# Optimization experiments

Hardware: AMD Instinct MI355X
Metric: run time of the kernel (lower is better)

Reference implementation:

```python
import jax, jax.numpy as jnp
import numpy as np

TOPK = 2
ALPHA_AUX = 0.02

def setup_inputs() -> dict:
    key = jax.random.key(0)
    ks = jax.random.split(key, 6)
    B, T, D, E, H = 2, 2048, 1024, 16, 1536
    s_in = 1.0 / np.sqrt(D)
    s_h = 1.0 / np.sqrt(H)
    return {
        "x": jax.random.normal(ks[0], (B, T, D), dtype=jnp.float32),
        "router_w": jax.random.normal(ks[1], (E, D), dtype=jnp.float32) * s_in,
        "w1": jax.random.normal(ks[2], (E, H, D), dtype=jnp.float32) * s_in,
        "b1": jax.random.normal(ks[3], (E, H), dtype=jnp.float32) * 0.01,
        "w2": jax.random.normal(ks[4], (E, D, H), dtype=jnp.float32) * s_h,
        "b2": jax.random.normal(ks[5], (E, D), dtype=jnp.float32) * 0.01,
    }

def reference(x, router_w, w1, b1, w2, b2):
    B, T, D = x.shape
    E = router_w.shape[0]
    N = B * T
    x_flat = x.reshape(N, D)

    # Router: top-k logits -> softmax gates -> dense dispatch matrix [N, E]
    logits = x_flat @ router_w.T                      # [N, E]
    vals, idx = jax.lax.top_k(logits, TOPK)           # [N, K]
    gate = jax.nn.softmax(vals, axis=-1)              # [N, K]
    rows = jnp.arange(N)[:, None]
    dispatch = jnp.zeros((N, E), dtype=x.dtype).at[rows, idx].set(gate)

    # Expert MLPs computed densely over all experts; gate==0 masks unselected,
    # reproducing the gather-MLP-scatter math exactly.
    h = jnp.einsum('nd,ehd->neh', x_flat, w1) + b1    # [N, E, H]
    h = jax.nn.gelu(h, approximate=True)              # tanh GELU
    y = jnp.einsum('neh,edh->ned', h, w2) + b2        # [N, E, D]
    out = jnp.einsum('ne,ned->nd', dispatch, y).reshape(B, T, D)

    # Auxiliary load-balancing loss
    tok_per_expert = (dispatch > 0).sum(0).astype(jnp.float32)  # [E]
    f_i = tok_per_expert / tok_per_expert.sum()
    m_i = dispatch.sum(0) / jnp.clip(tok_per_expert, 1.0, None)
    aux_loss = ALPHA_AUX * (f_i * m_i).mean()
    return out, aux_loss
```

## Files before the change

### kernel.cpp

```cpp
#include <hip/hip_runtime.h>
#include <hip/hip_bf16.h>
#include <math.h>

#define N_TOK 4096
#define DIM   1024
#define NEXP  16
#define HID   1536
#define TOPK2 2
#define NASSIGN (N_TOK * TOPK2)

#define MAX_ITEMS 80

typedef __attribute__((ext_vector_type(8))) short short8;
typedef __attribute__((ext_vector_type(4))) float floatx4;
typedef unsigned short u16;

#define GLOAD_LDS16(gp, lp)                                                     \
    __builtin_amdgcn_global_load_lds(                                           \
        (const __attribute__((address_space(1))) unsigned int*)(gp),            \
        (__attribute__((address_space(3))) unsigned int*)(lp), 16, 0, 0)

__global__ void cvt_kernel(const float* __restrict__ src, u16* __restrict__ dst, int n4) {
    int i = blockIdx.x * 256 + threadIdx.x;
    if (i >= n4) return;
    float4 v = ((const float4*)src)[i];
    __hip_bfloat16 a = __float2bfloat16(v.x), b = __float2bfloat16(v.y);
    __hip_bfloat16 c = __float2bfloat16(v.z), d = __float2bfloat16(v.w);
    ushort4 o;
    o.x = *(u16*)&a; o.y = *(u16*)&b; o.z = *(u16*)&c; o.w = *(u16*)&d;
    ((ushort4*)dst)[i] = o;
}

__global__ __launch_bounds__(256)
void logits_topk_kernel(const float* __restrict__ x, const float* __restrict__ rw,
                        int* __restrict__ idx, float* __restrict__ gate,
                        u16* __restrict__ x_bf) {
    int tb = blockIdx.x * 16;
    __shared__ float xs[16][68];
    __shared__ float rs[16][68];
    __shared__ float lg[16][17];

    int tid = threadIdx.x;
    int t = tid >> 4, e = tid & 15;
    int srow = tid >> 4, scol = (tid & 15) * 4;

    float acc = 0.f;
    for (int k0 = 0; k0 < DIM; k0 += 64) {
        float4 xv = *(const float4*)&x[(size_t)(tb + srow) * DIM + k0 + scol];
        *(float4*)&xs[srow][scol] = xv;
        *(float4*)&rs[srow][scol] = *(const float4*)&rw[(size_t)srow * DIM + k0 + scol];
        {
            __hip_bfloat16 a = __float2bfloat16(xv.x), b = __float2bfloat16(xv.y);
            __hip_bfloat16 c = __float2bfloat16(xv.z), d = __float2bfloat16(xv.w);
            ushort4 o;
            o.x = *(u16*)&a; o.y = *(u16*)&b; o.z = *(u16*)&c; o.w = *(u16*)&d;
            *(ushort4*)&x_bf[(size_t)(tb + srow) * DIM + k0 + scol] = o;
        }
        __syncthreads();
        const float2* xp = (const float2*)xs[t];
        const float2* rp = (const float2*)rs[e];
        #pragma unroll
        for (int k = 0; k < 32; k++) {
            float2 a = xp[k], b = rp[k];
            acc = fmaf(a.x, b.x, acc);
            acc = fmaf(a.y, b.y, acc);
        }
        __syncthreads();
    }
    lg[t][e] = acc;
    __syncthreads();

    if (tid < 16) {
        int n = tb + tid;
        float v0 = -3.402823466e+38f, v1 = -3.402823466e+38f;
        int i0 = 0, i1 = 0;
        #pragma unroll
        for (int ee = 0; ee < NEXP; ee++) {
            float v = lg[tid][ee];
            if (v > v0) { v1 = v0; i1 = i0; v0 = v; i0 = ee; }
            else if (v > v1) { v1 = v; i1 = ee; }
        }
        float e1 = expf(v1 - v0);
        float inv = 1.f / (1.f + e1);
        idx[2 * n] = i0; idx[2 * n + 1] = i1;
        gate[2 * n] = inv; gate[2 * n + 1] = e1 * inv;
    }
}

__global__ __launch_bounds__(256)
void plan_kernel(const int* __restrict__ idx, const float* __restrict__ gate,
                 int* __restrict__ offsets, int* __restrict__ tlist,
                 int* __restrict__ wl, int* __restrict__ wcount,
                 float* __restrict__ aux_out) {
    __shared__ int cnt_s[16];
    __shared__ float gs_s[16];
    __shared__ int pos_s[16];
    __shared__ int offs_s[17];
    int tid = threadIdx.x;
    if (tid < 16) { cnt_s[tid] = 0; gs_s[tid] = 0.f; pos_s[tid] = 0; }
    __syncthreads();
    for (int i = tid; i < NASSIGN; i += 256) {
        int e = idx[i];
        atomicAdd(&cnt_s[e], 1);
        atomicAdd(&gs_s[e], gate[i]);
    }
    __syncthreads();
    if (tid == 0) {
        int acc = 0;
        for (int e = 0; e < NEXP; e++) { offs_s[e] = acc; acc += cnt_s[e]; }
        offs_s[NEXP] = acc;
        float tot = (float)acc;
        float s = 0.f;
        for (int e = 0; e < NEXP; e++) {
            float c = (float)cnt_s[e];
            s += (c / tot) * (gs_s[e] / fmaxf(c, 1.f));
        }
        *aux_out = 0.02f * (s / (float)NEXP);
        int m = 0;
        for (int e = 0; e < NEXP; e++) {
            int nt = (cnt_s[e] + 127) >> 7;
            for (int rt = 0; rt < nt; rt++) wl[m++] = (e << 8) | rt;
        }
        *wcount = m;
    }
    __syncthreads();
    if (tid < 17) offsets[tid] = offs_s[tid];
    for (int i = tid; i < NASSIGN; i += 256) {
        int e = idx[i];
        int p = atomicAdd(&pos_s[e], 1);
        tlist[offs_s[e] + p] = i;
    }
}

__device__ __forceinline__ float gelu_tanh(float v) {
    float v3 = v * v * v;
    float t = tanhf(0.7978845608028654f * (v + 0.044715f * v3));
    return 0.5f * v * (1.f + t);
}


__global__ __launch_bounds__(256)
void gemm1_kernel(const u16* __restrict__ xb, const u16* __restrict__ w1b,
                  const float* __restrict__ b1,
                  const int* __restrict__ offsets, const int* __restrict__ tlist,
                  const int* __restrict__ wl, const int* __restrict__ wcount,
                  u16* __restrict__ h_bf) {
    int bid = blockIdx.x;
    int item = bid / 12;
    if (item >= *wcount) return;
    int colt = bid - item * 12;
    int w = wl[item];
    int e = w >> 8, rt = w & 255;
    int beg = offsets[e], ne = offsets[e + 1] - beg;
    int row0 = rt * 128, col0 = colt * 128;

    __shared__ u16 As[2][128 * 32];
    __shared__ u16 Bs[2][128 * 32];

    int tid = threadIdx.x;
    int wave = tid >> 6, lane = tid & 63;
    int wm = wave & 1, wn = wave >> 1;

    int koff = (((lane & 3) ^ ((lane >> 3) & 3)) * 8);
    const u16* aptr[2];
    const u16* bptr[2];
    #pragma unroll
    for (int q = 0; q < 2; q++) {
        int lrow = wave * 32 + q * 16 + (lane >> 2);
        int gi = beg + row0 + lrow;
        int gi2 = (row0 + lrow < ne) ? gi : beg;
        int tok = tlist[gi2] >> 1;
        aptr[q] = xb + (size_t)tok * DIM + koff;
        int n = col0 + lrow;
        bptr[q] = w1b + (size_t)(e * HID + n) * DIM + koff;
    }

    int rchunk = (((lane >> 4) ^ ((lane >> 1) & 3)) * 8);

    floatx4 acc[4][4] = {};
    #pragma unroll
    for (int q = 0; q < 2; q++) {
        GLOAD_LDS16(aptr[q], &As[0][(wave * 32 + q * 16) * 32]);
        GLOAD_LDS16(bptr[q], &Bs[0][(wave * 32 + q * 16) * 32]);
    }
    __syncthreads();
    int cur = 0;
    for (int k0 = 0; k0 < DIM; k0 += 32) {
        if (k0 + 32 < DIM) {
            #pragma unroll
            for (int q = 0; q < 2; q++) {
                GLOAD_LDS16(aptr[q] + k0 + 32, &As[cur ^ 1][(wave * 32 + q * 16) * 32]);
                GLOAD_LDS16(bptr[q] + k0 + 32, &Bs[cur ^ 1][(wave * 32 + q * 16) * 32]);
            }
        }
        short8 af[4], bf_[4];
        #pragma unroll
        for (int mi = 0; mi < 4; mi++)
            af[mi] = *(const short8*)&As[cur][(wm * 64 + mi * 16 + (lane & 15)) * 32 + rchunk];
        #pragma unroll
        for (int nj = 0; nj < 4; nj++)
            bf_[nj] = *(const short8*)&Bs[cur][(wn * 64 + nj * 16 + (lane & 15)) * 32 + rchunk];
        #pragma unroll
        for (int mi = 0; mi < 4; mi++)
            #pragma unroll
            for (int nj = 0; nj < 4; nj++)
                acc[mi][nj] = __builtin_amdgcn_mfma_f32_16x16x32_bf16(af[mi], bf_[nj], acc[mi][nj], 0, 0, 0);
        __syncthreads();
        cur ^= 1;
    }

    #pragma unroll
    for (int mi = 0; mi < 4; mi++) {
        #pragma unroll
        for (int r = 0; r < 4; r++) {
            int lrow = wm * 64 + mi * 16 + (lane >> 4) * 4 + r;
            if (row0 + lrow >= ne) continue;
            size_t orow = (size_t)(beg + row0 + lrow);
            #pragma unroll
            for (int nj = 0; nj < 4; nj++) {
                int col = col0 + wn * 64 + nj * 16 + (lane & 15);
                float v = acc[mi][nj][r] + b1[e * HID + col];
                __hip_bfloat16 hb = __float2bfloat16(gelu_tanh(v));
                h_bf[orow * HID + col] = *(u16*)&hb;
            }
        }
    }
}

__global__ __launch_bounds__(256)
void gemm2_kernel(const u16* __restrict__ h_bf, const u16* __restrict__ w2b,
                  const float* __restrict__ b2,
                  const int* __restrict__ offsets, const int* __restrict__ tlist,
                  const int* __restrict__ wl, const int* __restrict__ wcount,
                  const float* __restrict__ gate, float* __restrict__ out) {
    int bid = blockIdx.x;
    int item = bid >> 4;
    if (item >= *wcount) return;
    int colt = bid & 7;
    int ks = (bid >> 3) & 1;
    int w = wl[item];
    int e = w >> 8, rt = w & 255;
    int beg = offsets[e], ne = offsets[e + 1] - beg;
    int row0 = rt * 128, col0 = colt * 128;
    int kbeg = ks * (HID / 2);
    int kend = kbeg + (HID / 2);

    __shared__ u16 As[2][128 * 32];
    __shared__ u16 Bs[2][128 * 32];

    int tid = threadIdx.x;
    int wave = tid >> 6, lane = tid & 63;
    int wm = wave & 1, wn = wave >> 1;

    int koff = (((lane & 3) ^ ((lane >> 3) & 3)) * 8);
    const u16* aptr[2];
    const u16* bptr[2];
    #pragma unroll
    for (int q = 0; q < 2; q++) {
        int lrow = wave * 32 + q * 16 + (lane >> 2);
        int gi = beg + row0 + lrow;
        int gi2 = (row0 + lrow < ne) ? gi : beg;
        aptr[q] = h_bf + (size_t)gi2 * HID + koff;
        int n = col0 + lrow;
        bptr[q] = w2b + (size_t)(e * DIM + n) * HID + koff;
    }

    int rchunk = (((lane >> 4) ^ ((lane >> 1) & 3)) * 8);

    floatx4 acc[4][4] = {};
    #pragma unroll
    for (int q = 0; q < 2; q++) {
        GLOAD_LDS16(aptr[q] + kbeg, &As[0][(wave * 32 + q * 16) * 32]);
        GLOAD_LDS16(bptr[q] + kbeg, &Bs[0][(wave * 32 + q * 16) * 32]);
    }
    __syncthreads();
    int cur = 0;
    for (int k0 = kbeg; k0 < kend; k0 += 32) {
        if (k0 + 32 < kend) {
            #pragma unroll
            for (int q = 0; q < 2; q++) {
                GLOAD_LDS16(aptr[q] + k0 + 32, &As[cur ^ 1][(wave * 32 + q * 16) * 32]);
                GLOAD_LDS16(bptr[q] + k0 + 32, &Bs[cur ^ 1][(wave * 32 + q * 16) * 32]);
            }
        }
        short8 af[4], bf_[4];
        #pragma unroll
        for (int mi = 0; mi < 4; mi++)
            af[mi] = *(const short8*)&As[cur][(wm * 64 + mi * 16 + (lane & 15)) * 32 + rchunk];
        #pragma unroll
        for (int nj = 0; nj < 4; nj++)
            bf_[nj] = *(const short8*)&Bs[cur][(wn * 64 + nj * 16 + (lane & 15)) * 32 + rchunk];
        #pragma unroll
        for (int mi = 0; mi < 4; mi++)
            #pragma unroll
            for (int nj = 0; nj < 4; nj++)
                acc[mi][nj] = __builtin_amdgcn_mfma_f32_16x16x32_bf16(af[mi], bf_[nj], acc[mi][nj], 0, 0, 0);
        __syncthreads();
        cur ^= 1;
    }

    #pragma unroll
    for (int mi = 0; mi < 4; mi++) {
        #pragma unroll
        for (int r = 0; r < 4; r++) {
            int lrow = wm * 64 + mi * 16 + (lane >> 4) * 4 + r;
            if (row0 + lrow >= ne) continue;
            int t = tlist[beg + row0 + lrow];
            float g = gate[t];
            int tok = t >> 1;
            #pragma unroll
            for (int nj = 0; nj < 4; nj++) {
                int col = col0 + wn * 64 + nj * 16 + (lane & 15);
                float v = acc[mi][nj][r];
                if (ks == 0) v += b2[e * DIM + col];
                v *= g;
                atomicAdd(&out[(size_t)tok * DIM + col], v);
            }
        }
    }
}

extern "C" void kernel_launch(void* const* d_in, const int* in_sizes, int n_in,
                              void* d_out, int out_size, void* d_ws, size_t ws_size,
                              hipStream_t stream) {
    const float* x  = (const float*)d_in[0];
    const float* rw = (const float*)d_in[1];
    const float* w1 = (const float*)d_in[2];
    const float* b1 = (const float*)d_in[3];
    const float* w2 = (const float*)d_in[4];
    const float* b2 = (const float*)d_in[5];
    float* out = (float*)d_out;

    char* ws = (char*)d_ws;
    int*   offsets = (int*)(ws + 192);
    int*   wcount  = (int*)(ws + 384);
    int*   wl      = (int*)(ws + 512);
    int*   idx     = (int*)(ws + 4096);
    float* gate    = (float*)(ws + 4096 + 4 * NASSIGN);
    int*   tlist   = (int*)(ws + 4096 + 8 * NASSIGN);
    u16*   x_bf    = (u16*)(ws + (128 << 10));
    u16*   h_bf    = x_bf + (size_t)N_TOK * DIM;
    u16*   w_bf    = h_bf + (size_t)NASSIGN * HID;

    hipMemsetAsync(d_out, 0, (size_t)out_size * 4, stream);

    cvt_kernel<<<(NEXP * HID * DIM / 4 + 255) / 256, 256, 0, stream>>>(w1, w_bf, NEXP * HID * DIM / 4);

    logits_topk_kernel<<<N_TOK / 16, 256, 0, stream>>>(x, rw, idx, gate, x_bf);
    plan_kernel<<<1, 256, 0, stream>>>(idx, gate, offsets, tlist, wl, wcount,
                                       out + (size_t)N_TOK * DIM);

    gemm1_kernel<<<MAX_ITEMS * 12, 256, 0, stream>>>(
        x_bf, w_bf, b1, offsets, tlist, wl, wcount, h_bf);

    cvt_kernel<<<(NEXP * DIM * HID / 4 + 255) / 256, 256, 0, stream>>>(w2, w_bf, NEXP * DIM * HID / 4);

    gemm2_kernel<<<MAX_ITEMS * 16, 256, 0, stream>>>(
        h_bf, w_bf, b2, offsets, tlist, wl, wcount, gate, out);
}
```

Baseline: 487.1 us.

## Fuse weight conversions into router/GEMM1 launches and replace atomic scatter with combine

Folds the w1 bf16 conversion into the router kernel and the w2 conversion into the GEMM1 launch as extra blocks, so conversion overlaps with compute and two launches go away. GEMM2 drops its split-K in favour of a full-K loop and writes gated per-slot rows to a float buffer. A new combine kernel then sums each token's two slots, which removes the output memset and the atomics. The cost is extra workspace (separate w1/w2 bf16 buffers plus a y buffer reusing w1's space), with a fallback to the old atomic path when the workspace is too small. GEMM2 now launches half as many blocks.

```diff
diff --git a/kernel.cpp b/kernel.cpp
--- a/kernel.cpp
+++ b/kernel.cpp
@@ -10,6 +10,9 @@
 #define NASSIGN (N_TOK * TOPK2)
 
 #define MAX_ITEMS 80
+#define G1_BLOCKS (MAX_ITEMS * 12)
+#define W_ELEMS   (NEXP * HID * DIM)
+#define CVT_BLOCKS (W_ELEMS / 4 / 256)
 
 typedef __attribute__((ext_vector_type(8))) short short8;
 typedef __attribute__((ext_vector_type(4))) float floatx4;
@@ -20,9 +23,8 @@
         (const __attribute__((address_space(1))) unsigned int*)(gp),            \
         (__attribute__((address_space(3))) unsigned int*)(lp), 16, 0, 0)
 
-__global__ void cvt_kernel(const float* __restrict__ src, u16* __restrict__ dst, int n4) {
-    int i = blockIdx.x * 256 + threadIdx.x;
-    if (i >= n4) return;
+__device__ __forceinline__ void cvt_one4(const float* __restrict__ src,
+                                         u16* __restrict__ dst, int i) {
     float4 v = ((const float4*)src)[i];
     __hip_bfloat16 a = __float2bfloat16(v.x), b = __float2bfloat16(v.y);
     __hip_bfloat16 c = __float2bfloat16(v.z), d = __float2bfloat16(v.w);
@@ -31,16 +33,28 @@
     ((ushort4*)dst)[i] = o;
 }
 
+__global__ void cvt_kernel(const float* __restrict__ src, u16* __restrict__ dst, int n4) {
+    int i = blockIdx.x * 256 + threadIdx.x;
+    if (i >= n4) return;
+    cvt_one4(src, dst, i);
+}
+
 __global__ __launch_bounds__(256)
-void logits_topk_kernel(const float* __restrict__ x, const float* __restrict__ rw,
-                        int* __restrict__ idx, float* __restrict__ gate,
-                        u16* __restrict__ x_bf) {
+void router_cvtw1_kernel(const float* __restrict__ x, const float* __restrict__ rw,
+                         int* __restrict__ idx, float* __restrict__ gate,
+                         u16* __restrict__ x_bf,
+                         const float* __restrict__ w1src, u16* __restrict__ w1dst) {
+    int tid = threadIdx.x;
+    if (blockIdx.x >= 256) {
+        int i = (blockIdx.x - 256) * 256 + tid;
+        cvt_one4(w1src, w1dst, i);
+        return;
+    }
     int tb = blockIdx.x * 16;
     __shared__ float xs[16][68];
     __shared__ float rs[16][68];
     __shared__ float lg[16][17];
 
-    int tid = threadIdx.x;
     int t = tid >> 4, e = tid & 15;
     int srow = tid >> 4, scol = (tid & 15) * 4;
 
@@ -90,6 +104,7 @@
 __global__ __launch_bounds__(256)
 void plan_kernel(const int* __restrict__ idx, const float* __restrict__ gate,
                  int* __restrict__ offsets, int* __restrict__ tlist,
+                 int* __restrict__ slot_of,
                  int* __restrict__ wl, int* __restrict__ wcount,
                  float* __restrict__ aux_out) {
     __shared__ int cnt_s[16];
@@ -128,7 +143,9 @@
     for (int i = tid; i < NASSIGN; i += 256) {
         int e = idx[i];
         int p = atomicAdd(&pos_s[e], 1);
-        tlist[offs_s[e] + p] = i;
+        int s = offs_s[e] + p;
+        tlist[s] = i;
+        slot_of[i] = s;
     }
 }
 
@@ -140,12 +157,19 @@
 
 
 __global__ __launch_bounds__(256)
-void gemm1_kernel(const u16* __restrict__ xb, const u16* __restrict__ w1b,
-                  const float* __restrict__ b1,
-                  const int* __restrict__ offsets, const int* __restrict__ tlist,
-                  const int* __restrict__ wl, const int* __restrict__ wcount,
-                  u16* __restrict__ h_bf) {
+void gemm1_cvtw2_kernel(const u16* __restrict__ xb, const u16* __restrict__ w1b,
+                        const float* __restrict__ b1,
+                        const int* __restrict__ offsets, const int* __restrict__ tlist,
+                        const int* __restrict__ wl, const int* __restrict__ wcount,
+                        u16* __restrict__ h_bf,
+                        const float* __restrict__ w2src, u16* __restrict__ w2dst) {
     int bid = blockIdx.x;
+    int tid = threadIdx.x;
+    if (bid >= G1_BLOCKS) {
+        int i = (bid - G1_BLOCKS) * 256 + tid;
+        cvt_one4(w2src, w2dst, i);
+        return;
+    }
     int item = bid / 12;
     if (item >= *wcount) return;
     int colt = bid - item * 12;
@@ -157,7 +181,6 @@
     __shared__ u16 As[2][128 * 32];
     __shared__ u16 Bs[2][128 * 32];
 
-    int tid = threadIdx.x;
     int wave = tid >> 6, lane = tid & 63;
     int wm = wave & 1, wn = wave >> 1;
 
@@ -232,18 +255,16 @@
                   const float* __restrict__ b2,
                   const int* __restrict__ offsets, const int* __restrict__ tlist,
                   const int* __restrict__ wl, const int* __restrict__ wcount,
-                  const float* __restrict__ gate, float* __restrict__ out) {
+                  const float* __restrict__ gate, float* __restrict__ ydst,
+                  int use_y) {
     int bid = blockIdx.x;
-    int item = bid >> 4;
+    int item = bid >> 3;
     if (item >= *wcount) return;
     int colt = bid & 7;
-    int ks = (bid >> 3) & 1;
     int w = wl[item];
     int e = w >> 8, rt = w & 255;
     int beg = offsets[e], ne = offsets[e + 1] - beg;
     int row0 = rt * 128, col0 = colt * 128;
-    int kbeg = ks * (HID / 2);
-    int kend = kbeg + (HID / 2);
 
     __shared__ u16 As[2][128 * 32];
     __shared__ u16 Bs[2][128 * 32];
@@ -270,13 +291,13 @@
     floatx4 acc[4][4] = {};
     #pragma unroll
     for (int q = 0; q < 2; q++) {
-        GLOAD_LDS16(aptr[q] + kbeg, &As[0][(wave * 32 + q * 16) * 32]);
-        GLOAD_LDS16(bptr[q] + kbeg, &Bs[0][(wave * 32 + q * 16) * 32]);
+        GLOAD_LDS16(aptr[q], &As[0][(wave * 32 + q * 16) * 32]);
+        GLOAD_LDS16(bptr[q], &Bs[0][(wave * 32 + q * 16) * 32]);
     }
     __syncthreads();
     int cur = 0;
-    for (int k0 = kbeg; k0 < kend; k0 += 32) {
-        if (k0 + 32 < kend) {
+    for (int k0 = 0; k0 < HID; k0 += 32) {
+        if (k0 + 32 < HID) {
             #pragma unroll
             for (int q = 0; q < 2; q++) {
                 GLOAD_LDS16(aptr[q] + k0 + 32, &As[cur ^ 1][(wave * 32 + q * 16) * 32]);
@@ -305,19 +326,40 @@
         for (int r = 0; r < 4; r++) {
             int lrow = wm * 64 + mi * 16 + (lane >> 4) * 4 + r;
             if (row0 + lrow >= ne) continue;
-            int t = tlist[beg + row0 + lrow];
+            int slot = beg + row0 + lrow;
+            int t = tlist[slot];
             float g = gate[t];
-            int tok = t >> 1;
-            #pragma unroll
-            for (int nj = 0; nj < 4; nj++) {
-                int col = col0 + wn * 64 + nj * 16 + (lane & 15);
-                float v = acc[mi][nj][r];
-                if (ks == 0) v += b2[e * DIM + col];
-                v *= g;
-                atomicAdd(&out[(size_t)tok * DIM + col], v);
+            if (use_y) {
+                #pragma unroll
+                for (int nj = 0; nj < 4; nj++) {
+                    int col = col0 + wn * 64 + nj * 16 + (lane & 15);
+                    float v = g * (acc[mi][nj][r] + b2[e * DIM + col]);
+                    ydst[(size_t)slot * DIM + col] = v;
+                }
+            } else {
+                int tok = t >> 1;
+                #pragma unroll
+                for (int nj = 0; nj < 4; nj++) {
+                    int col = col0 + wn * 64 + nj * 16 + (lane & 15);
+                    float v = g * (acc[mi][nj][r] + b2[e * DIM + col]);
+                    atomicAdd(&ydst[(size_t)tok * DIM + col], v);
+                }
             }
         }
     }
+}
+
+__global__ __launch_bounds__(256)
+void combine_kernel(const float* __restrict__ y, const int* __restrict__ slot_of,
+                    float* __restrict__ out) {
+    int t = blockIdx.x;
+    int c4 = threadIdx.x;
+    int s0 = slot_of[2 * t], s1 = slot_of[2 * t + 1];
+    float4 a = ((const float4*)(y + (size_t)s0 * DIM))[c4];
+    float4 b = ((const float4*)(y + (size_t)s1 * DIM))[c4];
+    float4 o;
+    o.x = a.x + b.x; o.y = a.y + b.y; o.z = a.z + b.z; o.w = a.w + b.w;
+    ((float4*)(out + (size_t)t * DIM))[c4] = o;
 }
 
 extern "C" void kernel_launch(void* const* d_in, const int* in_sizes, int n_in,
@@ -338,23 +380,41 @@
     int*   idx     = (int*)(ws + 4096);
     float* gate    = (float*)(ws + 4096 + 4 * NASSIGN);
     int*   tlist   = (int*)(ws + 4096 + 8 * NASSIGN);
-    u16*   x_bf    = (u16*)(ws + (128 << 10));
+    int*   slot_of = (int*)(ws + 4096 + 12 * NASSIGN);
+    u16*   x_bf    = (u16*)(ws + (256 << 10));
     u16*   h_bf    = x_bf + (size_t)N_TOK * DIM;
-    u16*   w_bf    = h_bf + (size_t)NASSIGN * HID;
-
-    hipMemsetAsync(d_out, 0, (size_t)out_size * 4, stream);
-
-    cvt_kernel<<<(NEXP * HID * DIM / 4 + 255) / 256, 256, 0, stream>>>(w1, w_bf, NEXP * HID * DIM / 4);
-
-    logits_topk_kernel<<<N_TOK / 16, 256, 0, stream>>>(x, rw, idx, gate, x_bf);
-    plan_kernel<<<1, 256, 0, stream>>>(idx, gate, offsets, tlist, wl, wcount,
-                                       out + (size_t)N_TOK * DIM);
-
-    gemm1_kernel<<<MAX_ITEMS * 12, 256, 0, stream>>>(
-        x_bf, w_bf, b1, offsets, tlist, wl, wcount, h_bf);
-
-    cvt_kernel<<<(NEXP * DIM * HID / 4 + 255) / 256, 256, 0, stream>>>(w2, w_bf, NEXP * DIM * HID / 4);
-
-    gemm2_kernel<<<MAX_ITEMS * 16, 256, 0, stream>>>(
-        h_bf, w_bf, b2, offsets, tlist, wl, wcount, gate, out);
-}
+    u16*   w1_bf   = h_bf + (size_t)NASSIGN * HID;
+    u16*   w2_bf   = w1_bf + (size_t)W_ELEMS;
+
+    const size_t NEED_FULL = (size_t)(256 << 10)
+                           + (size_t)N_TOK * DIM * 2
+                           + (size_t)NASSIGN * HID * 2
+                           + (size_t)W_ELEMS * 2 * 2;
+    int full = (ws_size >= NEED_FULL) ? 1 : 0;
+
+    if (full) {
+        float* y = (float*)w1_bf;
+
+        router_cvtw1_kernel<<<256 + CVT_BLOCKS, 256, 0, stream>>>(
+            x, rw, idx, gate, x_bf, w1, w1_bf);
+        plan_kernel<<<1, 256, 0, stream>>>(idx, gate, offsets, tlist, slot_of,
+                                           wl, wcount, out + (size_t)N_TOK * DIM);
+        gemm1_cvtw2_kernel<<<G1_BLOCKS + CVT_BLOCKS, 256, 0, stream>>>(
+            x_bf, w1_bf, b1, offsets, tlist, wl, wcount, h_bf, w2, w2_bf);
+        gemm2_kernel<<<MAX_ITEMS * 8, 256, 0, stream>>>(
+            h_bf, w2_bf, b2, offsets, tlist, wl, wcount, gate, y, 1);
+        combine_kernel<<<N_TOK, 256, 0, stream>>>(y, slot_of, out);
+    } else {
+        u16* w_bf = w1_bf;
+        hipMemsetAsync(d_out, 0, (size_t)out_size * 4, stream);
+        router_cvtw1_kernel<<<256 + CVT_BLOCKS, 256, 0, stream>>>(
+            x, rw, idx, gate, x_bf, w1, w_bf);
+        plan_kernel<<<1, 256, 0, stream>>>(idx, gate, offsets, tlist, slot_of,
+                                           wl, wcount, out + (size_t)N_TOK * DIM);
+        gemm1_cvtw2_kernel<<<G1_BLOCKS, 256, 0, stream>>>(
+            x_bf, w_bf, b1, offsets, tlist, wl, wcount, h_bf, w2, w_bf);
+        cvt_kernel<<<CVT_BLOCKS, 256, 0, stream>>>(w2, w_bf, W_ELEMS / 4);
+        gemm2_kernel<<<MAX_ITEMS * 8, 256, 0, stream>>>(
+            h_bf, w_bf, b2, offsets, tlist, wl, wcount, gate, out, 0);
+    }
+}
```

Result: faster. 402.7 us (-17.3%).
